# Kernel optimization log

Measured on AMD Instinct MI355X. Metric: run time of the kernel, lower is better.

## Reference

```python
import jax, jax.numpy as jnp
import numpy as np

SEQ, BATCH, HID, NLAYERS = 2048, 16, 1024, 2


def setup_inputs() -> dict:
    key = jax.random.key(0)
    ks = jax.random.split(key, 3)
    scale = 1.0 / np.sqrt(HID)
    x = jax.random.normal(ks[0], (SEQ, BATCH, HID), dtype=jnp.float32)
    W0 = jax.random.normal(ks[1], (HID, 3 * HID), dtype=jnp.float32) * scale
    b0 = jnp.zeros((2 * HID,), dtype=jnp.float32)
    W1 = jax.random.normal(ks[2], (HID, 3 * HID), dtype=jnp.float32) * scale
    b1 = jnp.zeros((2 * HID,), dtype=jnp.float32)
    return {"x": x, "W0": W0, "b0": b0, "W1": W1, "b1": b1}


def _sru_layer(x, W, b):
    # x: [L, B, H]; W: [H, 3H]; b: [2H]
    L, B, H = x.shape
    U = jnp.einsum('lbd,dk->lbk', x, W)  # [L, B, 3H]
    x_tilde = U[..., :H]
    bf, br = b[:H], b[H:]
    f = jax.nn.sigmoid(U[..., H:2 * H] + bf)  # forget gate [L,B,H]
    r = jax.nn.sigmoid(U[..., 2 * H:] + br)   # reset gate  [L,B,H]

    def step(c_prev, inp):
        xt_t, f_t = inp
        c_t = f_t * c_prev + (1.0 - f_t) * xt_t
        return c_t, c_t

    c0 = jnp.zeros((B, H), dtype=x.dtype)
    _, cs = jax.lax.scan(step, c0, (x_tilde, f))  # cs: [L, B, H]
    h = r * cs + (1.0 - r) * x  # highway connection
    return h


def reference(x, W0, b0, W1, b1):
    h = _sru_layer(x, W0, b0)
    h = _sru_layer(h, W1, b1)
    return h[-1:]  # [1, B, H], matching `out[-1:]`
```

## Files before the change

kernel.cpp:

```cpp
#include <hip/hip_runtime.h>

#define SEQ    2048
#define BATCH  16
#define HID    1024
#define M_TOT  (SEQ*BATCH)
#define NCH    (BATCH*HID)
#define NCHUNK 32
#define TCHUNK (SEQ/NCHUNK)

typedef __attribute__((ext_vector_type(8))) short          short8;
typedef __attribute__((ext_vector_type(8))) unsigned short ushort8_t;
typedef __attribute__((ext_vector_type(4))) float          floatx4;

__device__ __forceinline__ unsigned short f32_to_bf16(float f) {
  unsigned int u = __float_as_uint(f);
  u += 0x7FFFu + ((u >> 16) & 1u);
  return (unsigned short)(u >> 16);
}
__device__ __forceinline__ float bf16_to_f32(unsigned short h) {
  return __uint_as_float(((unsigned int)h) << 16);
}
__device__ __forceinline__ float sigmoidf_(float x) {
  return 1.f / (1.f + __expf(-x));
}

#define LDS_DMA16(gp, lp) \
  __builtin_amdgcn_global_load_lds((const __attribute__((address_space(1))) void*)(gp), \
                                   (__attribute__((address_space(3))) void*)(lp), 16, 0, 0)


__global__ void cast_swizzle_f32(const float* __restrict__ src, unsigned short* __restrict__ dst,
                                 int K) {
  __shared__ unsigned short tile[4096];
  const int mt = blockIdx.x, kt = blockIdx.y;
  const int t = threadIdx.x;
  const int r = t >> 1, kh = (t & 1) * 16;
  const float* sp = src + (size_t)(mt * 128 + r) * K + kt * 32 + kh;
  float4 v0 = *(const float4*)(sp + 0);
  float4 v1 = *(const float4*)(sp + 4);
  float4 v2 = *(const float4*)(sp + 8);
  float4 v3 = *(const float4*)(sp + 12);
  ushort8_t u0, u1;
  u0[0]=f32_to_bf16(v0.x); u0[1]=f32_to_bf16(v0.y); u0[2]=f32_to_bf16(v0.z); u0[3]=f32_to_bf16(v0.w);
  u0[4]=f32_to_bf16(v1.x); u0[5]=f32_to_bf16(v1.y); u0[6]=f32_to_bf16(v1.z); u0[7]=f32_to_bf16(v1.w);
  u1[0]=f32_to_bf16(v2.x); u1[1]=f32_to_bf16(v2.y); u1[2]=f32_to_bf16(v2.z); u1[3]=f32_to_bf16(v2.w);
  u1[4]=f32_to_bf16(v3.x); u1[5]=f32_to_bf16(v3.y); u1[6]=f32_to_bf16(v3.z); u1[7]=f32_to_bf16(v3.w);
  const int c = r >> 4, lr = r & 15, q0 = kh >> 3;
  const int unit0 = c * 64 + (q0 << 4) + lr;
  *(ushort8_t*)&tile[unit0 * 8]        = u0;
  *(ushort8_t*)&tile[(unit0 + 16) * 8] = u1;
  __syncthreads();
  const size_t base = ((size_t)mt * (K >> 5) + kt) * 4096;
  *(ushort8_t*)&dst[base + t * 16]     = *(const ushort8_t*)&tile[t * 16];
  *(ushort8_t*)&dst[base + t * 16 + 8] = *(const ushort8_t*)&tile[t * 16 + 8];
}

__global__ void swizzle_bf16(const unsigned short* __restrict__ src, unsigned short* __restrict__ dst,
                             int K) {
  __shared__ unsigned short tile[4096];
  const int mt = blockIdx.x, kt = blockIdx.y;
  const int t = threadIdx.x;
  const int r = t >> 1, kh = (t & 1) * 16;
  const unsigned short* sp = src + (size_t)(mt * 128 + r) * K + kt * 32 + kh;
  ushort8_t u0 = *(const ushort8_t*)(sp + 0);
  ushort8_t u1 = *(const ushort8_t*)(sp + 8);
  const int c = r >> 4, lr = r & 15, q0 = kh >> 3;
  const int unit0 = c * 64 + (q0 << 4) + lr;
  *(ushort8_t*)&tile[unit0 * 8]        = u0;
  *(ushort8_t*)&tile[(unit0 + 16) * 8] = u1;
  __syncthreads();
  const size_t base = ((size_t)mt * (K >> 5) + kt) * 4096;
  *(ushort8_t*)&dst[base + t * 16]     = *(const ushort8_t*)&tile[t * 16];
  *(ushort8_t*)&dst[base + t * 16 + 8] = *(const ushort8_t*)&tile[t * 16 + 8];
}

__global__ void w_prep(const float* __restrict__ W, unsigned short* __restrict__ Wsw) {
  __shared__ unsigned short tile[4096];
  const int nt = blockIdx.x, kt = blockIdx.y;
  const int t = threadIdx.x;
  const int kk = t >> 3, n0 = (t & 7) * 16;
  const float* sp = W + (size_t)(kt * 32 + kk) * 3072 + nt * 128 + n0;
  float v[16];
#pragma unroll
  for (int i = 0; i < 16; i += 4) {
    float4 f = *(const float4*)(sp + i);
    v[i] = f.x; v[i+1] = f.y; v[i+2] = f.z; v[i+3] = f.w;
  }
  const int cbase = (n0 >> 4) * 64 + ((kk >> 3) << 4);
#pragma unroll
  for (int j = 0; j < 16; j++)
    tile[(cbase + j) * 8 + (kk & 7)] = f32_to_bf16(v[j]);
  __syncthreads();
  const size_t base = ((size_t)nt * 32 + kt) * 4096;
  *(ushort8_t*)&Wsw[base + t * 16]     = *(const ushort8_t*)&tile[t * 16];
  *(ushort8_t*)&Wsw[base + t * 16 + 8] = *(const ushort8_t*)&tile[t * 16 + 8];
}

__global__ __launch_bounds__(256, 4) void gemm_sw_fused(
    const unsigned short* __restrict__ A, const unsigned short* __restrict__ B,
    unsigned short* __restrict__ Xt, unsigned short* __restrict__ Fo, unsigned short* __restrict__ Ro,
    const float* __restrict__ bias, int NBN)
{
  __shared__ __align__(16) unsigned short As[2][4096];
  __shared__ __align__(16) unsigned short Bs[2][4096];
  const int tid = threadIdx.x;
  const int wave = tid >> 6, lane = tid & 63;
  const int id = blockIdx.x;
  const int xcd = id & 7, slot = id >> 3;
  const int NB8 = NBN << 3;
  const int g    = slot / NB8;
  const int rem  = slot - g * NB8;
  const int bn   = rem >> 3;
  const int bm   = xcd * 32 + g * 8 + (rem & 7);
  const int wm = wave >> 1, wn = wave & 1;

  const int so = wave * 1024 + lane * 8;
  const unsigned short* gA = A + (size_t)bm * 32 * 4096 + so;
  const unsigned short* gB = B + (size_t)bn * 32 * 4096 + so;
  const int l0 = wave * 1024;

  floatx4 acc[4][4];
#pragma unroll
  for (int i = 0; i < 4; i++)
#pragma unroll
    for (int j = 0; j < 4; j++)
#pragma unroll
      for (int r = 0; r < 4; r++) acc[i][j][r] = 0.f;

  const int ra = wm * 2048 + lane * 8;
  const int rb = wn * 2048 + lane * 8;

  auto stage = [&](int buf) {
    LDS_DMA16(gA,       As[buf] + l0);
    LDS_DMA16(gA + 512, As[buf] + l0 + 512);
    LDS_DMA16(gB,       Bs[buf] + l0);
    LDS_DMA16(gB + 512, Bs[buf] + l0 + 512);
    gA += 4096; gB += 4096;
  };
  auto compute = [&](int buf) {
    short8 a[4], b[4];
#pragma unroll
    for (int i = 0; i < 4; i++) a[i] = *(const short8*)(As[buf] + ra + i * 512);
#pragma unroll
    for (int j = 0; j < 4; j++) b[j] = *(const short8*)(Bs[buf] + rb + j * 512);
#pragma unroll
    for (int i = 0; i < 4; i++)
#pragma unroll
      for (int j = 0; j < 4; j++)
        acc[i][j] = __builtin_amdgcn_mfma_f32_16x16x32_bf16(a[i], b[j], acc[i][j], 0, 0, 0);
  };

  stage(0);
#pragma unroll 1
  for (int kt = 0; kt < 32; kt += 2) {
    __syncthreads();
    stage(1);
    compute(0);
    __syncthreads();
    if (kt + 2 < 32) stage(0);
    compute(1);
  }

  const int region = bn >> 3;
  const int colb = (bn & 7) * 128 + wn * 64 + (lane & 15);
  const int row0 = bm * 128 + wm * 64 + ((lane >> 4) << 2);
  if (region == 0) {
#pragma unroll
    for (int i = 0; i < 4; i++)
#pragma unroll
      for (int j = 0; j < 4; j++)
#pragma unroll
        for (int rg = 0; rg < 4; rg++)
          Xt[(size_t)(row0 + i * 16 + rg) * 1024 + colb + j * 16] = f32_to_bf16(acc[i][j][rg]);
  } else {
    unsigned short* O = (region == 1) ? Fo : Ro;
    const float* bp = bias + (region - 1) * 1024;
#pragma unroll
    for (int j = 0; j < 4; j++) {
      float bb = bp[colb + j * 16];
#pragma unroll
      for (int i = 0; i < 4; i++)
#pragma unroll
        for (int rg = 0; rg < 4; rg++) {
          float s = sigmoidf_(acc[i][j][rg] + bb);
          O[(size_t)(row0 + i * 16 + rg) * 1024 + colb + j * 16] = f32_to_bf16(s);
        }
    }
  }
}

__global__ void scan_pass1(const unsigned short* __restrict__ Xt, const unsigned short* __restrict__ F,
                           float* __restrict__ P, float* __restrict__ S) {
  int ch = blockIdx.x * blockDim.x + threadIdx.x;
  int chunk = blockIdx.y;
  size_t idx = (size_t)chunk * TCHUNK * NCH + ch;
  float p = 1.f, s = 0.f;
  for (int t = 0; t < TCHUNK; ++t) {
    float f  = bf16_to_f32(F[idx]);
    float xt = bf16_to_f32(Xt[idx]);
    s = f * s + (1.f - f) * xt;
    p *= f;
    idx += NCH;
  }
  P[(size_t)chunk * NCH + ch] = p;
  S[(size_t)chunk * NCH + ch] = s;
}

__global__ void combine_c0(const float* __restrict__ P, const float* __restrict__ S,
                           float* __restrict__ C0) {
  int ch = blockIdx.x * blockDim.x + threadIdx.x;
  float c = 0.f;
  for (int k = 0; k < NCHUNK; ++k) {
    C0[(size_t)k * NCH + ch] = c;
    c = P[(size_t)k * NCH + ch] * c + S[(size_t)k * NCH + ch];
  }
}

__global__ void scan1_pass2(const unsigned short* __restrict__ Xt, const unsigned short* __restrict__ F,
                            const unsigned short* __restrict__ R, const unsigned short* __restrict__ xsw,
                            const float* __restrict__ C0, unsigned short* __restrict__ h1b) {
  int ch = blockIdx.x * blockDim.x + threadIdx.x;
  int chunk = blockIdx.y;
  const int b = ch >> 10, h = ch & 1023;
  float c = C0[(size_t)chunk * NCH + ch];
  size_t idx = (size_t)chunk * TCHUNK * NCH + ch;
  const int hblk = h >> 5;
  const int lsub = ((h >> 3) & 3) * 16 + b;
  const int h7 = h & 7;
  for (int tt = 0; tt < TCHUNK; ++tt) {
    const int t = chunk * TCHUNK + tt;
    float f  = bf16_to_f32(F[idx]);
    float xt = bf16_to_f32(Xt[idx]);
    c = f * c + (1.f - f) * xt;
    float r  = bf16_to_f32(R[idx]);
    size_t soff = ((size_t)(t >> 3) * 32 + hblk) * 4096
                + (size_t)(((t & 7) * 64 + lsub) * 8 + h7);
    float xv = bf16_to_f32(xsw[soff]);
    h1b[idx] = f32_to_bf16(r * c + (1.f - r) * xv);
    idx += NCH;
  }
}

__global__ void r2_kernel(const unsigned short* __restrict__ h1b, const float* __restrict__ W1,
                          const float* __restrict__ b1, float* __restrict__ r2) {
  __shared__ float xrow[1024];
  const int b = blockIdx.x, nq = blockIdx.y, tid = threadIdx.x;
  for (int i = tid; i < 1024; i += 256)
    xrow[i] = bf16_to_f32(h1b[(size_t)(2047 * 16 + b) * 1024 + i]);
  __syncthreads();
  const int n = nq * 256 + tid;
  float acc = b1[1024 + n];
  for (int d = 0; d < 1024; ++d)
    acc += xrow[d] * W1[(size_t)d * 3072 + 2048 + n];
  r2[b * 1024 + n] = sigmoidf_(acc);
}

__global__ void combine_final(const float* __restrict__ P, const float* __restrict__ S,
                              const float* __restrict__ r2, const unsigned short* __restrict__ h1b,
                              float* __restrict__ out) {
  int ch = blockIdx.x * blockDim.x + threadIdx.x;
  float c = 0.f;
  for (int k = 0; k < NCHUNK; ++k)
    c = P[(size_t)k * NCH + ch] * c + S[(size_t)k * NCH + ch];
  float r = r2[ch];
  float x = bf16_to_f32(h1b[(size_t)2047 * NCH + ch]);
  out[ch] = r * c + (1.f - r) * x;
}

extern "C" void kernel_launch(void* const* d_in, const int* in_sizes, int n_in,
                              void* d_out, int out_size, void* d_ws, size_t ws_size,
                              hipStream_t stream) {
  const float* x  = (const float*)d_in[0];
  const float* W0 = (const float*)d_in[1];
  const float* b0 = (const float*)d_in[2];
  const float* W1 = (const float*)d_in[3];
  const float* b1 = (const float*)d_in[4];
  float* out = (float*)d_out;

  char* ws = (char*)d_ws;
  auto alloc = [&](size_t bytes) {
    char* p = ws; ws += (bytes + 255) & ~(size_t)255; return p;
  };
  const size_t NE = (size_t)M_TOT * HID;
  unsigned short* xsw   = (unsigned short*)alloc(NE * 2);
  unsigned short* W0sw  = (unsigned short*)alloc((size_t)3072 * 1024 * 2);
  unsigned short* W1sw  = (unsigned short*)alloc((size_t)3072 * 1024 * 2);
  unsigned short* Xt    = (unsigned short*)alloc(NE * 2);
  unsigned short* F     = (unsigned short*)alloc(NE * 2);
  unsigned short* R     = (unsigned short*)alloc(NE * 2);
  unsigned short* h1b   = (unsigned short*)alloc(NE * 2);
  unsigned short* h1sw  = (unsigned short*)alloc(NE * 2);
  float* P   = (float*)alloc((size_t)NCHUNK * NCH * 4);
  float* S   = (float*)alloc((size_t)NCHUNK * NCH * 4);
  float* C0  = (float*)alloc((size_t)NCHUNK * NCH * 4);
  float* r2  = (float*)alloc((size_t)NCH * 4);

  dim3 blk256(256);
  cast_swizzle_f32<<<dim3(M_TOT / 128, 32), blk256, 0, stream>>>(x, xsw, 1024);
  w_prep<<<dim3(24, 32), blk256, 0, stream>>>(W0, W0sw);
  w_prep<<<dim3(24, 32), blk256, 0, stream>>>(W1, W1sw);
  gemm_sw_fused<<<dim3(24 * 256), blk256, 0, stream>>>(xsw, W0sw, Xt, F, R, b0, 24);
  scan_pass1<<<dim3(NCH / 256, NCHUNK), blk256, 0, stream>>>(Xt, F, P, S);
  combine_c0<<<dim3(NCH / 256), blk256, 0, stream>>>(P, S, C0);
  scan1_pass2<<<dim3(NCH / 256, NCHUNK), blk256, 0, stream>>>(Xt, F, R, xsw, C0, h1b);
  swizzle_bf16<<<dim3(M_TOT / 128, 32), blk256, 0, stream>>>(h1b, h1sw, 1024);
  gemm_sw_fused<<<dim3(16 * 256), blk256, 0, stream>>>(h1sw, W1sw, Xt, F, R, b1, 16);
  r2_kernel<<<dim3(16, 4), blk256, 0, stream>>>(h1b, W1, b1, r2);
  scan_pass1<<<dim3(NCH / 256, NCHUNK), blk256, 0, stream>>>(Xt, F, P, S);
  combine_final<<<dim3(NCH / 256), blk256, 0, stream>>>(P, S, r2, h1b, out);
}
```

Before: 838.5 us.

## Fuse prep kernels, vectorize scans, write swizzled h1 directly from scan

Merges the three input/weight prep kernels into one launch. Vectorizes the scan, combine and final kernels so each thread handles 8 channels with 16-byte loads. Fuses the second scan pass with the bf16 swizzle by staging outputs in LDS and writing the GEMM-ready layout directly, which removes the h1b round trip and a separate kernel, and keeps only the last timestep for r2/final. The trade-off is far fewer threads (only 256 blocks) in the scan kernels, which may hurt latency hiding.

```diff
diff --git a/kernel.cpp b/kernel.cpp
--- a/kernel.cpp
+++ b/kernel.cpp
@@ -29,13 +29,11 @@
                                    (__attribute__((address_space(3))) void*)(lp), 16, 0, 0)
 
 
-__global__ void cast_swizzle_f32(const float* __restrict__ src, unsigned short* __restrict__ dst,
-                                 int K) {
+__device__ __forceinline__ void cast_swizzle_body(const float* __restrict__ src,
+    unsigned short* __restrict__ dst, int mt, int kt, int t) {
   __shared__ unsigned short tile[4096];
-  const int mt = blockIdx.x, kt = blockIdx.y;
-  const int t = threadIdx.x;
   const int r = t >> 1, kh = (t & 1) * 16;
-  const float* sp = src + (size_t)(mt * 128 + r) * K + kt * 32 + kh;
+  const float* sp = src + (size_t)(mt * 128 + r) * 1024 + kt * 32 + kh;
   float4 v0 = *(const float4*)(sp + 0);
   float4 v1 = *(const float4*)(sp + 4);
   float4 v2 = *(const float4*)(sp + 8);
@@ -50,34 +48,14 @@
   *(ushort8_t*)&tile[unit0 * 8]        = u0;
   *(ushort8_t*)&tile[(unit0 + 16) * 8] = u1;
   __syncthreads();
-  const size_t base = ((size_t)mt * (K >> 5) + kt) * 4096;
+  const size_t base = ((size_t)mt * 32 + kt) * 4096;
   *(ushort8_t*)&dst[base + t * 16]     = *(const ushort8_t*)&tile[t * 16];
   *(ushort8_t*)&dst[base + t * 16 + 8] = *(const ushort8_t*)&tile[t * 16 + 8];
 }
 
-__global__ void swizzle_bf16(const unsigned short* __restrict__ src, unsigned short* __restrict__ dst,
-                             int K) {
+__device__ __forceinline__ void w_prep_body(const float* __restrict__ W,
+    unsigned short* __restrict__ Wsw, int nt, int kt, int t) {
   __shared__ unsigned short tile[4096];
-  const int mt = blockIdx.x, kt = blockIdx.y;
-  const int t = threadIdx.x;
-  const int r = t >> 1, kh = (t & 1) * 16;
-  const unsigned short* sp = src + (size_t)(mt * 128 + r) * K + kt * 32 + kh;
-  ushort8_t u0 = *(const ushort8_t*)(sp + 0);
-  ushort8_t u1 = *(const ushort8_t*)(sp + 8);
-  const int c = r >> 4, lr = r & 15, q0 = kh >> 3;
-  const int unit0 = c * 64 + (q0 << 4) + lr;
-  *(ushort8_t*)&tile[unit0 * 8]        = u0;
-  *(ushort8_t*)&tile[(unit0 + 16) * 8] = u1;
-  __syncthreads();
-  const size_t base = ((size_t)mt * (K >> 5) + kt) * 4096;
-  *(ushort8_t*)&dst[base + t * 16]     = *(const ushort8_t*)&tile[t * 16];
-  *(ushort8_t*)&dst[base + t * 16 + 8] = *(const ushort8_t*)&tile[t * 16 + 8];
-}
-
-__global__ void w_prep(const float* __restrict__ W, unsigned short* __restrict__ Wsw) {
-  __shared__ unsigned short tile[4096];
-  const int nt = blockIdx.x, kt = blockIdx.y;
-  const int t = threadIdx.x;
   const int kk = t >> 3, n0 = (t & 7) * 16;
   const float* sp = W + (size_t)(kt * 32 + kk) * 3072 + nt * 128 + n0;
   float v[16];
@@ -94,6 +72,16 @@
   const size_t base = ((size_t)nt * 32 + kt) * 4096;
   *(ushort8_t*)&Wsw[base + t * 16]     = *(const ushort8_t*)&tile[t * 16];
   *(ushort8_t*)&Wsw[base + t * 16 + 8] = *(const ushort8_t*)&tile[t * 16 + 8];
+}
+
+__global__ __launch_bounds__(256) void prep_all(const float* __restrict__ x,
+    const float* __restrict__ W0, const float* __restrict__ W1,
+    unsigned short* __restrict__ xsw, unsigned short* __restrict__ W0sw,
+    unsigned short* __restrict__ W1sw) {
+  const int id = blockIdx.x, t = threadIdx.x;
+  if (id < 8192)        cast_swizzle_body(x, xsw, id >> 5, id & 31, t);
+  else if (id < 8960)   w_prep_body(W0, W0sw, (id - 8192) >> 5, (id - 8192) & 31, t);
+  else                  w_prep_body(W1, W1sw, (id - 8960) >> 5, (id - 8960) & 31, t);
 }
 
 __global__ __launch_bounds__(256, 4) void gemm_sw_fused(
@@ -189,64 +177,121 @@
   }
 }
 
-__global__ void scan_pass1(const unsigned short* __restrict__ Xt, const unsigned short* __restrict__ F,
-                           float* __restrict__ P, float* __restrict__ S) {
-  int ch = blockIdx.x * blockDim.x + threadIdx.x;
-  int chunk = blockIdx.y;
+__global__ __launch_bounds__(256) void scan_pass1(
+    const unsigned short* __restrict__ Xt, const unsigned short* __restrict__ F,
+    float* __restrict__ P, float* __restrict__ S) {
+  const int ch = (blockIdx.x * 256 + threadIdx.x) * 8;
+  const int chunk = blockIdx.y;
   size_t idx = (size_t)chunk * TCHUNK * NCH + ch;
-  float p = 1.f, s = 0.f;
+  float p[8], s[8];
+#pragma unroll
+  for (int j = 0; j < 8; j++) { p[j] = 1.f; s[j] = 0.f; }
   for (int t = 0; t < TCHUNK; ++t) {
-    float f  = bf16_to_f32(F[idx]);
-    float xt = bf16_to_f32(Xt[idx]);
-    s = f * s + (1.f - f) * xt;
-    p *= f;
+    ushort8_t fv = *(const ushort8_t*)&F[idx];
+    ushort8_t xv = *(const ushort8_t*)&Xt[idx];
+#pragma unroll
+    for (int j = 0; j < 8; j++) {
+      float f  = bf16_to_f32(fv[j]);
+      float xt = bf16_to_f32(xv[j]);
+      s[j] = f * s[j] + (1.f - f) * xt;
+      p[j] *= f;
+    }
     idx += NCH;
   }
-  P[(size_t)chunk * NCH + ch] = p;
-  S[(size_t)chunk * NCH + ch] = s;
-}
-
-__global__ void combine_c0(const float* __restrict__ P, const float* __restrict__ S,
-                           float* __restrict__ C0) {
-  int ch = blockIdx.x * blockDim.x + threadIdx.x;
-  float c = 0.f;
+  float4* P4 = (float4*)&P[(size_t)chunk * NCH + ch];
+  float4* S4 = (float4*)&S[(size_t)chunk * NCH + ch];
+  P4[0] = make_float4(p[0], p[1], p[2], p[3]);
+  P4[1] = make_float4(p[4], p[5], p[6], p[7]);
+  S4[0] = make_float4(s[0], s[1], s[2], s[3]);
+  S4[1] = make_float4(s[4], s[5], s[6], s[7]);
+}
+
+__global__ __launch_bounds__(256) void combine_c0(
+    const float* __restrict__ P, const float* __restrict__ S, float* __restrict__ C0) {
+  const int ch = (blockIdx.x * 256 + threadIdx.x) * 8;
+  float c[8];
+#pragma unroll
+  for (int j = 0; j < 8; j++) c[j] = 0.f;
   for (int k = 0; k < NCHUNK; ++k) {
-    C0[(size_t)k * NCH + ch] = c;
-    c = P[(size_t)k * NCH + ch] * c + S[(size_t)k * NCH + ch];
-  }
-}
-
-__global__ void scan1_pass2(const unsigned short* __restrict__ Xt, const unsigned short* __restrict__ F,
-                            const unsigned short* __restrict__ R, const unsigned short* __restrict__ xsw,
-                            const float* __restrict__ C0, unsigned short* __restrict__ h1b) {
-  int ch = blockIdx.x * blockDim.x + threadIdx.x;
-  int chunk = blockIdx.y;
-  const int b = ch >> 10, h = ch & 1023;
-  float c = C0[(size_t)chunk * NCH + ch];
+    float4* O4 = (float4*)&C0[(size_t)k * NCH + ch];
+    O4[0] = make_float4(c[0], c[1], c[2], c[3]);
+    O4[1] = make_float4(c[4], c[5], c[6], c[7]);
+    const float4* P4 = (const float4*)&P[(size_t)k * NCH + ch];
+    const float4* S4 = (const float4*)&S[(size_t)k * NCH + ch];
+    float4 p0 = P4[0], p1 = P4[1], s0 = S4[0], s1 = S4[1];
+    c[0] = p0.x*c[0]+s0.x; c[1] = p0.y*c[1]+s0.y; c[2] = p0.z*c[2]+s0.z; c[3] = p0.w*c[3]+s0.w;
+    c[4] = p1.x*c[4]+s1.x; c[5] = p1.y*c[5]+s1.y; c[6] = p1.z*c[6]+s1.z; c[7] = p1.w*c[7]+s1.w;
+  }
+}
+
+#define TPAD 4112
+__global__ __launch_bounds__(256) void scan1_pass2_fused(
+    const unsigned short* __restrict__ Xt, const unsigned short* __restrict__ F,
+    const unsigned short* __restrict__ R, const unsigned short* __restrict__ xsw,
+    const float* __restrict__ C0, unsigned short* __restrict__ h1sw,
+    unsigned short* __restrict__ h1last)
+{
+  __shared__ unsigned short st[4 * TPAD];
+  const int hb = blockIdx.x;
+  const int chunk = blockIdx.y;
+  const int tid = threadIdx.x;
+  const int b = tid >> 4, hg = tid & 15;
+  const int h0 = hb * 128 + hg * 8;
+  const int ch = b * 1024 + h0;
+  const int tl   = hg >> 2;
+  const int usub = (hg & 3) * 16 + b;
+
+  float c[8];
+  {
+    const float4* C4 = (const float4*)&C0[(size_t)chunk * NCH + ch];
+    float4 a = C4[0], d = C4[1];
+    c[0]=a.x; c[1]=a.y; c[2]=a.z; c[3]=a.w; c[4]=d.x; c[5]=d.y; c[6]=d.z; c[7]=d.w;
+  }
+
   size_t idx = (size_t)chunk * TCHUNK * NCH + ch;
-  const int hblk = h >> 5;
-  const int lsub = ((h >> 3) & 3) * 16 + b;
-  const int h7 = h & 7;
-  for (int tt = 0; tt < TCHUNK; ++tt) {
-    const int t = chunk * TCHUNK + tt;
-    float f  = bf16_to_f32(F[idx]);
-    float xt = bf16_to_f32(Xt[idx]);
-    c = f * c + (1.f - f) * xt;
-    float r  = bf16_to_f32(R[idx]);
-    size_t soff = ((size_t)(t >> 3) * 32 + hblk) * 4096
-                + (size_t)(((t & 7) * 64 + lsub) * 8 + h7);
-    float xv = bf16_to_f32(xsw[soff]);
-    h1b[idx] = f32_to_bf16(r * c + (1.f - r) * xv);
-    idx += NCH;
-  }
-}
-
-__global__ void r2_kernel(const unsigned short* __restrict__ h1b, const float* __restrict__ W1,
-                          const float* __restrict__ b1, float* __restrict__ r2) {
+  for (int t8 = 0; t8 < 8; ++t8) {
+#pragma unroll
+    for (int ts = 0; ts < 8; ++ts) {
+      const int t = chunk * TCHUNK + t8 * 8 + ts;
+      ushort8_t fv = *(const ushort8_t*)&F[idx];
+      ushort8_t xv = *(const ushort8_t*)&Xt[idx];
+      ushort8_t rv = *(const ushort8_t*)&R[idx];
+      const size_t soff = ((size_t)(t >> 3) * 32 + (h0 >> 5)) * 4096
+                        + (size_t)(((t & 7) * 64 + usub) * 8);
+      ushort8_t xo = *(const ushort8_t*)&xsw[soff];
+      ushort8_t hv;
+#pragma unroll
+      for (int j = 0; j < 8; ++j) {
+        float f  = bf16_to_f32(fv[j]);
+        float xt = bf16_to_f32(xv[j]);
+        c[j] = f * c[j] + (1.f - f) * xt;
+        float r  = bf16_to_f32(rv[j]);
+        float xval = bf16_to_f32(xo[j]);
+        hv[j] = f32_to_bf16(r * c[j] + (1.f - r) * xval);
+      }
+      *(ushort8_t*)&st[tl * TPAD + (ts * 64 + usub) * 8] = hv;
+      if (t == SEQ - 1) *(ushort8_t*)&h1last[ch] = hv;
+      idx += NCH;
+    }
+    __syncthreads();
+    const size_t gbase = (((size_t)chunk * 8 + t8) * 32 + hb * 4) * 4096;
+#pragma unroll
+    for (int tl2 = 0; tl2 < 4; ++tl2) {
+      size_t gdst = gbase + (size_t)tl2 * 4096 + tid * 16;
+      *(ushort8_t*)&h1sw[gdst]     = *(const ushort8_t*)&st[tl2 * TPAD + tid * 16];
+      *(ushort8_t*)&h1sw[gdst + 8] = *(const ushort8_t*)&st[tl2 * TPAD + tid * 16 + 8];
+    }
+    __syncthreads();
+  }
+}
+
+__global__ __launch_bounds__(256) void r2_kernel(
+    const unsigned short* __restrict__ h1last, const float* __restrict__ W1,
+    const float* __restrict__ b1, float* __restrict__ r2) {
   __shared__ float xrow[1024];
   const int b = blockIdx.x, nq = blockIdx.y, tid = threadIdx.x;
   for (int i = tid; i < 1024; i += 256)
-    xrow[i] = bf16_to_f32(h1b[(size_t)(2047 * 16 + b) * 1024 + i]);
+    xrow[i] = bf16_to_f32(h1last[b * 1024 + i]);
   __syncthreads();
   const int n = nq * 256 + tid;
   float acc = b1[1024 + n];
@@ -255,16 +300,32 @@
   r2[b * 1024 + n] = sigmoidf_(acc);
 }
 
-__global__ void combine_final(const float* __restrict__ P, const float* __restrict__ S,
-                              const float* __restrict__ r2, const unsigned short* __restrict__ h1b,
-                              float* __restrict__ out) {
-  int ch = blockIdx.x * blockDim.x + threadIdx.x;
-  float c = 0.f;
-  for (int k = 0; k < NCHUNK; ++k)
-    c = P[(size_t)k * NCH + ch] * c + S[(size_t)k * NCH + ch];
-  float r = r2[ch];
-  float x = bf16_to_f32(h1b[(size_t)2047 * NCH + ch]);
-  out[ch] = r * c + (1.f - r) * x;
+__global__ __launch_bounds__(256) void combine_final(
+    const float* __restrict__ P, const float* __restrict__ S,
+    const float* __restrict__ r2, const unsigned short* __restrict__ h1last,
+    float* __restrict__ out) {
+  const int ch = (blockIdx.x * 256 + threadIdx.x) * 8;
+  float c[8];
+#pragma unroll
+  for (int j = 0; j < 8; j++) c[j] = 0.f;
+  for (int k = 0; k < NCHUNK; ++k) {
+    const float4* P4 = (const float4*)&P[(size_t)k * NCH + ch];
+    const float4* S4 = (const float4*)&S[(size_t)k * NCH + ch];
+    float4 p0 = P4[0], p1 = P4[1], s0 = S4[0], s1 = S4[1];
+    c[0] = p0.x*c[0]+s0.x; c[1] = p0.y*c[1]+s0.y; c[2] = p0.z*c[2]+s0.z; c[3] = p0.w*c[3]+s0.w;
+    c[4] = p1.x*c[4]+s1.x; c[5] = p1.y*c[5]+s1.y; c[6] = p1.z*c[6]+s1.z; c[7] = p1.w*c[7]+s1.w;
+  }
+  const float4* R4 = (const float4*)&r2[ch];
+  float4 r0 = R4[0], r1 = R4[1];
+  ushort8_t hx = *(const ushort8_t*)&h1last[ch];
+  float o[8];
+  float rr[8] = {r0.x, r0.y, r0.z, r0.w, r1.x, r1.y, r1.z, r1.w};
+#pragma unroll
+  for (int j = 0; j < 8; j++)
+    o[j] = rr[j] * c[j] + (1.f - rr[j]) * bf16_to_f32(hx[j]);
+  float4* O4 = (float4*)&out[ch];
+  O4[0] = make_float4(o[0], o[1], o[2], o[3]);
+  O4[1] = make_float4(o[4], o[5], o[6], o[7]);
 }
 
 extern "C" void kernel_launch(void* const* d_in, const int* in_sizes, int n_in,
@@ -288,24 +349,21 @@
   unsigned short* Xt    = (unsigned short*)alloc(NE * 2);
   unsigned short* F     = (unsigned short*)alloc(NE * 2);
   unsigned short* R     = (unsigned short*)alloc(NE * 2);
-  unsigned short* h1b   = (unsigned short*)alloc(NE * 2);
   unsigned short* h1sw  = (unsigned short*)alloc(NE * 2);
+  unsigned short* h1last= (unsigned short*)alloc((size_t)NCH * 2);
   float* P   = (float*)alloc((size_t)NCHUNK * NCH * 4);
   float* S   = (float*)alloc((size_t)NCHUNK * NCH * 4);
   float* C0  = (float*)alloc((size_t)NCHUNK * NCH * 4);
   float* r2  = (float*)alloc((size_t)NCH * 4);
 
   dim3 blk256(256);
-  cast_swizzle_f32<<<dim3(M_TOT / 128, 32), blk256, 0, stream>>>(x, xsw, 1024);
-  w_prep<<<dim3(24, 32), blk256, 0, stream>>>(W0, W0sw);
-  w_prep<<<dim3(24, 32), blk256, 0, stream>>>(W1, W1sw);
+  prep_all<<<dim3(9728), blk256, 0, stream>>>(x, W0, W1, xsw, W0sw, W1sw);
   gemm_sw_fused<<<dim3(24 * 256), blk256, 0, stream>>>(xsw, W0sw, Xt, F, R, b0, 24);
-  scan_pass1<<<dim3(NCH / 256, NCHUNK), blk256, 0, stream>>>(Xt, F, P, S);
-  combine_c0<<<dim3(NCH / 256), blk256, 0, stream>>>(P, S, C0);
-  scan1_pass2<<<dim3(NCH / 256, NCHUNK), blk256, 0, stream>>>(Xt, F, R, xsw, C0, h1b);
-  swizzle_bf16<<<dim3(M_TOT / 128, 32), blk256, 0, stream>>>(h1b, h1sw, 1024);
+  scan_pass1<<<dim3(8, NCHUNK), blk256, 0, stream>>>(Xt, F, P, S);
+  combine_c0<<<dim3(8), blk256, 0, stream>>>(P, S, C0);
+  scan1_pass2_fused<<<dim3(8, NCHUNK), blk256, 0, stream>>>(Xt, F, R, xsw, C0, h1sw, h1last);
   gemm_sw_fused<<<dim3(16 * 256), blk256, 0, stream>>>(h1sw, W1sw, Xt, F, R, b1, 16);
-  r2_kernel<<<dim3(16, 4), blk256, 0, stream>>>(h1b, W1, b1, r2);
-  scan_pass1<<<dim3(NCH / 256, NCHUNK), blk256, 0, stream>>>(Xt, F, P, S);
-  combine_final<<<dim3(NCH / 256), blk256, 0, stream>>>(P, S, r2, h1b, out);
-}
+  r2_kernel<<<dim3(16, 4), blk256, 0, stream>>>(h1last, W1, b1, r2);
+  scan_pass1<<<dim3(8, NCHUNK), blk256, 0, stream>>>(Xt, F, P, S);
+  combine_final<<<dim3(8), blk256, 0, stream>>>(P, S, r2, h1last, out);
+}
```

After: 843.4 us. No clear change (+0.6%).
